# Kernel optimization log

Measured on AMD Instinct MI355X. Metric: run time of the kernel, lower is better.

Reference implementation:

```python
import jax, jax.numpy as jnp
import numpy as np

WIDTH = 1024
HEADS = 16
INIT_SCALE = 0.02


def setup_inputs() -> dict:
    key = jax.random.key(0)
    ks = jax.random.split(key, 5)
    x = jax.random.normal(ks[0], (2, 2048, WIDTH), dtype=jnp.float32)
    # torch Linear weight [out, in]; we store transposed [in, out] for x @ W
    W_qkv = jax.random.normal(ks[1], (WIDTH, 3 * WIDTH), dtype=jnp.float32) * INIT_SCALE
    b_qkv = jnp.zeros((3 * WIDTH,), dtype=jnp.float32)
    W_proj = jax.random.normal(ks[2], (WIDTH, WIDTH), dtype=jnp.float32) * INIT_SCALE
    b_proj = jnp.zeros((WIDTH,), dtype=jnp.float32)
    return {"x": x, "W_qkv": W_qkv, "b_qkv": b_qkv, "W_proj": W_proj, "b_proj": b_proj}


def reference(x, W_qkv, b_qkv, W_proj, b_proj):
    bs, n_ctx, width = x.shape
    heads = HEADS
    attn_ch = width // heads  # per-head channel dim (width*3 // heads // 3)
    scale = 1.0 / np.sqrt(np.sqrt(attn_ch))  # applied to both q and k

    qkv = x @ W_qkv + b_qkv                      # [b, t, 3*width]
    qkv = qkv.reshape(bs, n_ctx, heads, 3 * attn_ch)
    q, k, v = jnp.split(qkv, 3, axis=-1)         # each [b, t, h, c]

    weight = jnp.einsum('bthc,bshc->bhts', q * scale, k * scale)
    wdtype = weight.dtype
    weight = jax.nn.softmax(weight.astype(jnp.float32), axis=-1).astype(wdtype)

    out = jnp.einsum('bhts,bshc->bthc', weight, v).reshape(bs, n_ctx, width)
    return out @ W_proj + b_proj
```

## Files before the change

### kernel.cpp

```cpp
#include <hip/hip_runtime.h>

typedef __attribute__((ext_vector_type(4))) float fx4;
typedef __attribute__((ext_vector_type(16))) float f32x16;
typedef __attribute__((ext_vector_type(8))) short s16x8;
typedef __attribute__((ext_vector_type(2))) unsigned int u32x2;

#define QK_SCALE 0.35355339059327373f
#define LOG2E    1.4426950408889634f

__device__ __forceinline__ short f2bf(float f) {
  union { float f; unsigned int u; } v; v.f = f;
  unsigned int r = v.u + 0x7fffu + ((v.u >> 16) & 1u);
  return (short)(r >> 16);
}

__device__ __forceinline__ unsigned f2u(float f) {
  union { float f; unsigned u; } v; v.f = f; return v.u;
}
__device__ __forceinline__ float u2f(unsigned u) {
  union { unsigned u; float f; } v; v.u = u; return v.f;
}

__device__ __forceinline__ float xhalf_sum(float x) {
  u32x2 r = __builtin_amdgcn_permlane32_swap(f2u(x), f2u(x), false, false);
  return u2f(r[0]) + u2f(r[1]);
}

__device__ __forceinline__ int swz(int row, int cb) {
  return (row * 128 + cb) ^ ((row & 7) << 4);
}

#define GLL(g, lds) __builtin_amdgcn_global_load_lds( \
    (__attribute__((address_space(1))) void*)(void*)(g), \
    (__attribute__((address_space(3))) void*)(void*)(lds), 16, 0, 0)

__global__ __launch_bounds__(256) void prep(
    const float* __restrict__ x, short* __restrict__ x16,
    const float* __restrict__ Wqkv, short* __restrict__ WqkvT,
    const float* __restrict__ Wproj, short* __restrict__ WprojT) {
  const int b = blockIdx.x;
  if (b < 4096) {
    int i = b * 256 + threadIdx.x;
    float4 v = reinterpret_cast<const float4*>(x)[i];
    short4 o;
    o.x = f2bf(v.x); o.y = f2bf(v.y); o.z = f2bf(v.z); o.w = f2bf(v.w);
    reinterpret_cast<short4*>(x16)[i] = o;
    return;
  }
  __shared__ float tile[32][33];
  const float* W; short* WT; int N, bx, by;
  if (b < 7168) { W = Wqkv; WT = WqkvT; N = 3072; int r = b - 4096; bx = r % 96; by = r / 96; }
  else          { W = Wproj; WT = WprojT; N = 1024; int r = b - 7168; bx = r % 32; by = r / 32; }
  const int K = 1024;
  int tx = threadIdx.x & 31, ty = threadIdx.x >> 5;
  int n0 = bx * 32, k0 = by * 32;
#pragma unroll
  for (int i = 0; i < 32; i += 8)
    tile[ty + i][tx] = W[(size_t)(k0 + ty + i) * N + n0 + tx];
  __syncthreads();
#pragma unroll
  for (int i = 0; i < 32; i += 8)
    WT[(size_t)(n0 + ty + i) * K + k0 + tx] = f2bf(tile[tx][ty + i]);
}

template <int MODE, int BK, int BN>
__global__ __launch_bounds__(BN * 4, 4) void gemm_bf16(
    const short* __restrict__ A, const short* __restrict__ Bt,
    const float* __restrict__ bias, float* __restrict__ Cout,
    short* __restrict__ Qo, short* __restrict__ Ko, short* __restrict__ Vo,
    int M, int N, int K) {
  constexpr int T = BN * 4;
  constexpr int NWC = BN / 32;
  constexpr int CA = 16 * BK / T;
  constexpr int CB = BK / 32;
  __shared__ __align__(16) char sA[2][128 * BK * 2];
  __shared__ __align__(16) char sB[2][BN * BK * 2];
  const int tid = threadIdx.x;
  const int w = tid >> 6, l = tid & 63;
  const int lr = l & 15, lg = l >> 4;
  const int bid = blockIdx.x;
  const int m0 = ((bid & 7) * 4 + ((bid >> 3) & 3)) * 128;
  const int n0 = (bid >> 5) * BN;
  const int wr = (w / NWC) * 64, wc = (w % NWC) * 32;

  fx4 accT[2][4] = {};

  auto stage = [&](int kt, int buf) {
#pragma unroll
    for (int i = 0; i < CA; ++i) {
      int c = i * T + tid;
      int r, lch;
      if (BK == 64) { r = c >> 3; lch = (c & 7) ^ (r & 7); }
      else          { r = c >> 2; lch = (c & 3) ^ (r & 3); }
      GLL(A + (size_t)(m0 + r) * K + kt + lch * 8, sA[buf] + c * 16);
    }
#pragma unroll
    for (int i = 0; i < CB; ++i) {
      int c = i * T + tid;
      int r, lch;
      if (BK == 64) { r = c >> 3; lch = (c & 7) ^ (r & 7); }
      else          { r = c >> 2; lch = (c & 3) ^ (r & 3); }
      GLL(Bt + (size_t)(n0 + r) * K + kt + lch * 8, sB[buf] + c * 16);
    }
  };
  auto roff = [&](int R, int kk) {
    return (BK == 64) ? ((R * 128 + kk * 64 + lg * 16) ^ ((R & 7) << 4))
                      : ((R * 64 + lg * 16) ^ ((R & 3) << 4));
  };

  stage(0, 0);
  __syncthreads();

  const int NIT = K / BK;
  int cur = 0;
  for (int it = 0; it < NIT; ++it) {
    if (it + 1 < NIT) stage((it + 1) * BK, cur ^ 1);
#pragma unroll
    for (int kk = 0; kk < (BK == 64 ? 2 : 1); ++kk) {
      s16x8 av[4], bv[2];
#pragma unroll
      for (int m = 0; m < 4; ++m)
        av[m] = *reinterpret_cast<const s16x8*>(sA[cur] + roff(wr + m * 16 + lr, kk));
#pragma unroll
      for (int n = 0; n < 2; ++n)
        bv[n] = *reinterpret_cast<const s16x8*>(sB[cur] + roff(wc + n * 16 + lr, kk));
#pragma unroll
      for (int n = 0; n < 2; ++n)
#pragma unroll
        for (int m = 0; m < 4; ++m)
          accT[n][m] = __builtin_amdgcn_mfma_f32_16x16x32_bf16(bv[n], av[m], accT[n][m], 0, 0, 0);
    }
    __syncthreads();
    cur ^= 1;
  }

#pragma unroll
  for (int n = 0; n < 2; ++n) {
    const int col0 = n0 + wc + n * 16 + lg * 4;
    const float4 bs = *reinterpret_cast<const float4*>(bias + col0);
    if (MODE == 1) {
#pragma unroll
      for (int m = 0; m < 4; ++m) {
        int row = m0 + wr + m * 16 + lr;
        float4 v;
        v.x = accT[n][m][0] + bs.x; v.y = accT[n][m][1] + bs.y;
        v.z = accT[n][m][2] + bs.z; v.w = accT[n][m][3] + bs.w;
        *reinterpret_cast<float4*>(Cout + (size_t)row * N + col0) = v;
      }
    } else {
      const int h = col0 / 192;
      const int rr = col0 - h * 192;
#pragma unroll
      for (int m = 0; m < 4; ++m) {
        int row = m0 + wr + m * 16 + lr;
        int b = row >> 11, t = row & 2047;
        size_t bh = (size_t)b * 16 + h;
        float v0 = accT[n][m][0] + bs.x, v1 = accT[n][m][1] + bs.y;
        float v2 = accT[n][m][2] + bs.z, v3 = accT[n][m][3] + bs.w;
        if (rr < 64) {
          short4 s4;
          s4.x = f2bf(v0 * (QK_SCALE * LOG2E)); s4.y = f2bf(v1 * (QK_SCALE * LOG2E));
          s4.z = f2bf(v2 * (QK_SCALE * LOG2E)); s4.w = f2bf(v3 * (QK_SCALE * LOG2E));
          *reinterpret_cast<short4*>(Qo + (bh * 2048 + t) * 64 + rr) = s4;
        } else if (rr < 128) {
          short4 s4;
          s4.x = f2bf(v0 * QK_SCALE); s4.y = f2bf(v1 * QK_SCALE);
          s4.z = f2bf(v2 * QK_SCALE); s4.w = f2bf(v3 * QK_SCALE);
          *reinterpret_cast<short4*>(Ko + (bh * 2048 + t) * 64 + (rr - 64)) = s4;
        } else {
          Vo[(bh * 64 + (rr - 128) + 0) * 2048 + t] = f2bf(v0);
          Vo[(bh * 64 + (rr - 128) + 1) * 2048 + t] = f2bf(v1);
          Vo[(bh * 64 + (rr - 128) + 2) * 2048 + t] = f2bf(v2);
          Vo[(bh * 64 + (rr - 128) + 3) * 2048 + t] = f2bf(v3);
        }
      }
    }
  }
}

__global__ __launch_bounds__(512, 4) void attn_fwd(
    const short* __restrict__ Q, const short* __restrict__ Kc,
    const short* __restrict__ VT, short* __restrict__ Y) {
  __shared__ __align__(16) char smem[65536];
  const int tid = threadIdx.x;
  const int w = tid >> 6;
  const int wq = w & 3;
  const int half = w >> 2;
  const int t8 = tid & 255;
  const int l = tid & 63;
  const int l31 = l & 31, hi = l >> 5;
  const int bid = blockIdx.x;
  const int bh = (bid & 7) * 4 + ((bid >> 3) & 3);
  const int qt = bid >> 5;
  const int q0 = qt * 128 + wq * 32;
  const int sbase = half * 1024;

  char* kbase = smem + half * 16384;
  char* vbase = smem + 32768 + half * 16384;

  s16x8 qf[4];
  const short* qp = Q + ((size_t)bh * 2048 + q0 + l31) * 64 + hi * 8;
#pragma unroll
  for (int ks = 0; ks < 4; ++ks)
    qf[ks] = *reinterpret_cast<const s16x8*>(qp + ks * 16);

  float lsum = 0.f;
  f32x16 o0 = {}, o1 = {};

#pragma unroll
  for (int i = 0; i < 2; ++i) {
    int c = i * 256 + t8, r = c >> 3, pch = c & 7, lch = pch ^ (r & 7);
    GLL(Kc + ((size_t)bh * 2048 + sbase + r) * 64 + lch * 8, kbase + c * 16);
    GLL(VT + ((size_t)bh * 64 + r) * 2048 + sbase + lch * 8, vbase + c * 16);
  }
  __syncthreads();

  for (int sb = 0; sb < 16; ++sb) {
    const int s0 = sbase + sb * 64;
    if (sb < 15) {
      char* kn = kbase + ((sb + 1) & 1) * 8192;
      char* vn = vbase + ((sb + 1) & 1) * 8192;
#pragma unroll
      for (int i = 0; i < 2; ++i) {
        int c = i * 256 + t8, r = c >> 3, pch = c & 7, lch = pch ^ (r & 7);
        GLL(Kc + ((size_t)bh * 2048 + s0 + 64 + r) * 64 + lch * 8, kn + c * 16);
        GLL(VT + ((size_t)bh * 64 + r) * 2048 + s0 + 64 + lch * 8, vn + c * 16);
      }
    }
    const char* kb = kbase + (sb & 1) * 8192;
    const char* vb = vbase + (sb & 1) * 8192;

    f32x16 p0 = {}, p1 = {};
    __builtin_amdgcn_s_setprio(1);
#pragma unroll
    for (int ks = 0; ks < 4; ++ks) {
      int off = swz(l31, ks * 32 + hi * 16);
      s16x8 ka0 = *reinterpret_cast<const s16x8*>(kb + off);
      s16x8 ka1 = *reinterpret_cast<const s16x8*>(kb + off + 4096);
      p0 = __builtin_amdgcn_mfma_f32_32x32x16_bf16(ka0, qf[ks], p0, 0, 0, 0);
      p1 = __builtin_amdgcn_mfma_f32_32x32x16_bf16(ka1, qf[ks], p1, 0, 0, 0);
    }
    __builtin_amdgcn_s_setprio(0);

#pragma unroll
    for (int i = 0; i < 16; ++i) {
      p0[i] = __builtin_amdgcn_exp2f(p0[i]);
      p1[i] = __builtin_amdgcn_exp2f(p1[i]);
    }
    float s8[8];
#pragma unroll
    for (int i = 0; i < 8; ++i)
      s8[i] = (p0[2 * i] + p0[2 * i + 1]) + (p1[2 * i] + p1[2 * i + 1]);
    lsum += ((s8[0] + s8[1]) + (s8[2] + s8[3])) + ((s8[4] + s8[5]) + (s8[6] + s8[7]));

    int wd[16];
#pragma unroll
    for (int i = 0; i < 8; ++i) {
      asm("v_cvt_pk_bf16_f32 %0, %1, %2" : "=v"(wd[i]) : "v"(p0[2 * i]), "v"(p0[2 * i + 1]));
      asm("v_cvt_pk_bf16_f32 %0, %1, %2" : "=v"(wd[8 + i]) : "v"(p1[2 * i]), "v"(p1[2 * i + 1]));
    }

    __builtin_amdgcn_s_setprio(1);
#pragma unroll
    for (int t = 0; t < 4; ++t) {
      u32x2 s02 = __builtin_amdgcn_permlane32_swap(
          (unsigned)wd[4 * t], (unsigned)wd[4 * t + 2], false, false);
      u32x2 s13 = __builtin_amdgcn_permlane32_swap(
          (unsigned)wd[4 * t + 1], (unsigned)wd[4 * t + 3], false, false);
      union { unsigned i4[4]; s16x8 v; } fr;
      fr.i4[0] = s02[0]; fr.i4[1] = s13[0]; fr.i4[2] = s02[1]; fr.i4[3] = s13[1];
      int off = swz(l31, t * 32 + hi * 16);
      s16x8 v0 = *reinterpret_cast<const s16x8*>(vb + off);
      s16x8 v1 = *reinterpret_cast<const s16x8*>(vb + off + 4096);
      o0 = __builtin_amdgcn_mfma_f32_32x32x16_bf16(v0, fr.v, o0, 0, 0, 0);
      o1 = __builtin_amdgcn_mfma_f32_32x32x16_bf16(v1, fr.v, o1, 0, 0, 0);
    }
    __builtin_amdgcn_s_setprio(0);
    __syncthreads();
  }

  float lt = xhalf_sum(lsum);
  float* scr = (float*)smem;
  float* slsum = (float*)(smem + 32768);
  if (half == 1) {
    float* op = scr + wq * 2048;
#pragma unroll
    for (int gq = 0; gq < 4; ++gq)
#pragma unroll
      for (int j = 0; j < 4; ++j) {
        op[(hi * 4 + 8 * gq + j) * 32 + l31] = o0[4 * gq + j];
        op[(32 + hi * 4 + 8 * gq + j) * 32 + l31] = o1[4 * gq + j];
      }
    if (hi == 0) slsum[wq * 32 + l31] = lt;
  }
  __syncthreads();
  if (half == 0) {
    const int b = bh >> 4, h = bh & 15;
    float inv = 1.f / (lt + slsum[wq * 32 + l31]);
    const float* op = scr + wq * 2048;
    short* yp = Y + ((size_t)b * 2048 + q0 + l31) * 1024 + h * 64 + hi * 4;
#pragma unroll
    for (int gq = 0; gq < 4; ++gq) {
      short4 s4;
      s4.x = f2bf((o0[4 * gq + 0] + op[(hi * 4 + 8 * gq + 0) * 32 + l31]) * inv);
      s4.y = f2bf((o0[4 * gq + 1] + op[(hi * 4 + 8 * gq + 1) * 32 + l31]) * inv);
      s4.z = f2bf((o0[4 * gq + 2] + op[(hi * 4 + 8 * gq + 2) * 32 + l31]) * inv);
      s4.w = f2bf((o0[4 * gq + 3] + op[(hi * 4 + 8 * gq + 3) * 32 + l31]) * inv);
      *reinterpret_cast<short4*>(yp + 8 * gq) = s4;
      s4.x = f2bf((o1[4 * gq + 0] + op[(32 + hi * 4 + 8 * gq + 0) * 32 + l31]) * inv);
      s4.y = f2bf((o1[4 * gq + 1] + op[(32 + hi * 4 + 8 * gq + 1) * 32 + l31]) * inv);
      s4.z = f2bf((o1[4 * gq + 2] + op[(32 + hi * 4 + 8 * gq + 2) * 32 + l31]) * inv);
      s4.w = f2bf((o1[4 * gq + 3] + op[(32 + hi * 4 + 8 * gq + 3) * 32 + l31]) * inv);
      *reinterpret_cast<short4*>(yp + 32 + 8 * gq) = s4;
    }
  }
}

extern "C" void kernel_launch(void* const* d_in, const int* in_sizes, int n_in,
                              void* d_out, int out_size, void* d_ws, size_t ws_size,
                              hipStream_t stream) {
  const float* x     = (const float*)d_in[0];
  const float* Wqkv  = (const float*)d_in[1];
  const float* bqkv  = (const float*)d_in[2];
  const float* Wproj = (const float*)d_in[3];
  const float* bproj = (const float*)d_in[4];
  float* out = (float*)d_out;

  char* ws = (char*)d_ws;
  const size_t MB = 1024 * 1024;
  short* x16    = (short*)(ws);
  short* WqkvT  = (short*)(ws + 8 * MB);
  short* WprojT = (short*)(ws + 14 * MB);
  short* Q16    = (short*)(ws + 16 * MB);
  short* K16    = (short*)(ws + 24 * MB);
  short* VT16   = (short*)(ws + 32 * MB);
  short* Y16    = x16;

  prep<<<8192, 256, 0, stream>>>(x, x16, Wqkv, WqkvT, Wproj, WprojT);
  gemm_bf16<0, 32, 128><<<768, 512, 0, stream>>>(x16, WqkvT, bqkv, nullptr,
                                                 Q16, K16, VT16, 4096, 3072, 1024);
  attn_fwd<<<512, 512, 0, stream>>>(Q16, K16, VT16, Y16);
  gemm_bf16<1, 64, 64><<<512, 256, 0, stream>>>(Y16, WprojT, bproj, out,
                                                nullptr, nullptr, nullptr, 4096, 1024, 1024);
}
```

Baseline: 110.1 us.

## Replace QKV GEMM with 256x256-tile, 4-stage async-copy pipelined kernel

Splits the QKV projection into a dedicated kernel using 256x256 output tiles with BK=32. It streams A and B through a 4-buffer ring in 128KB of dynamic LDS using direct global-to-LDS loads, with XOR swizzling and explicit vmcnt waits. Barriers and setprio are interleaved around the MFMA blocks to overlap loads with compute. The larger tiles raise operand reuse and cut global traffic, but only 192 blocks are launched on a 256-CU device, which risks underusing the GPU.

After: 117.1 us. +6.3%, slower.

```diff
diff --git a/kernel.cpp b/kernel.cpp
--- a/kernel.cpp
+++ b/kernel.cpp
@@ -63,11 +63,128 @@
     WT[(size_t)(n0 + ty + i) * K + k0 + tx] = f2bf(tile[tx][ty + i]);
 }
 
-template <int MODE, int BK, int BN>
-__global__ __launch_bounds__(BN * 4, 4) void gemm_bf16(
+__global__ __launch_bounds__(512, 2) void gemm_qkv(
+    const short* __restrict__ A, const short* __restrict__ Bt,
+    const float* __restrict__ bias,
+    short* __restrict__ Qo, short* __restrict__ Ko, short* __restrict__ Vo) {
+  constexpr int K = 1024;
+  extern __shared__ __align__(16) char smem[];
+  const int tid = threadIdx.x;
+  const int w = tid >> 6, l = tid & 63;
+  const int lr = l & 15, lg = l >> 4;
+  const int wm = w >> 2, wn = w & 3;
+  const int bid = blockIdx.x;
+  const int idx = (bid & 7) * 24 + (bid >> 3);
+  const int m0 = (idx & 15) * 256;
+  const int n0 = (idx >> 4) * 256;
+
+  fx4 accT[4][8] = {};
+
+  auto stageA = [&](int s) {
+    char* dst = smem + (s & 3) * 32768;
+#pragma unroll
+    for (int i = 0; i < 2; ++i) {
+      int c = i * 512 + tid, r = c >> 2, lch = (c & 3) ^ (r & 3);
+      GLL(A + (size_t)(m0 + r) * K + s * 32 + lch * 8, dst + c * 16);
+    }
+  };
+  auto stageB = [&](int s) {
+    char* dst = smem + (s & 3) * 32768 + 16384;
+#pragma unroll
+    for (int i = 0; i < 2; ++i) {
+      int c = i * 512 + tid, r = c >> 2, lch = (c & 3) ^ (r & 3);
+      GLL(Bt + (size_t)(n0 + r) * K + s * 32 + lch * 8, dst + c * 16);
+    }
+  };
+
+  for (int j = 0; j < 3; ++j) { stageA(j); stageB(j); }
+  asm volatile("s_waitcnt vmcnt(8)" ::: "memory");
+  __builtin_amdgcn_s_barrier();
+  __builtin_amdgcn_sched_barrier(0);
+
+  for (int s = 0; s < 32; ++s) {
+    const char* sa = smem + (s & 3) * 32768;
+    const char* sb = sa + 16384;
+    const bool st = (s + 3 < 32);
+    s16x8 bv[4];
+#pragma unroll
+    for (int mh = 0; mh < 2; ++mh) {
+      if (mh == 0) { if (st) stageA(s + 3); }
+      else         { if (st) stageB(s + 3); }
+      s16x8 av[4];
+#pragma unroll
+      for (int mi = 0; mi < 4; ++mi) {
+        int R = wm * 128 + mh * 64 + mi * 16 + lr;
+        av[mi] = *reinterpret_cast<const s16x8*>(sa + ((R * 64 + lg * 16) ^ ((R & 3) << 4)));
+      }
+      if (mh == 0) {
+#pragma unroll
+        for (int n = 0; n < 4; ++n) {
+          int R = wn * 64 + n * 16 + lr;
+          bv[n] = *reinterpret_cast<const s16x8*>(sb + ((R * 64 + lg * 16) ^ ((R & 3) << 4)));
+        }
+      }
+      __builtin_amdgcn_s_barrier();
+      __builtin_amdgcn_sched_barrier(0);
+      __builtin_amdgcn_s_setprio(1);
+#pragma unroll
+      for (int n = 0; n < 4; ++n)
+#pragma unroll
+        for (int mi = 0; mi < 4; ++mi)
+          accT[n][mh * 4 + mi] = __builtin_amdgcn_mfma_f32_16x16x32_bf16(
+              bv[n], av[mi], accT[n][mh * 4 + mi], 0, 0, 0);
+      __builtin_amdgcn_s_setprio(0);
+      if (mh == 0) {
+        __builtin_amdgcn_s_barrier();
+        __builtin_amdgcn_sched_barrier(0);
+      }
+    }
+    if (s < 31) {
+      if (s <= 28)      asm volatile("s_waitcnt vmcnt(8)" ::: "memory");
+      else if (s == 29) asm volatile("s_waitcnt vmcnt(4)" ::: "memory");
+      else              asm volatile("s_waitcnt vmcnt(0)" ::: "memory");
+      __builtin_amdgcn_s_barrier();
+      __builtin_amdgcn_sched_barrier(0);
+    }
+  }
+
+#pragma unroll
+  for (int n = 0; n < 4; ++n) {
+    const int col0 = n0 + wn * 64 + n * 16 + lg * 4;
+    const float4 bs = *reinterpret_cast<const float4*>(bias + col0);
+    const int h = col0 / 192;
+    const int rr = col0 - h * 192;
+#pragma unroll
+    for (int m = 0; m < 8; ++m) {
+      int row = m0 + wm * 128 + m * 16 + lr;
+      int b = row >> 11, t = row & 2047;
+      size_t bh = (size_t)b * 16 + h;
+      float v0 = accT[n][m][0] + bs.x, v1 = accT[n][m][1] + bs.y;
+      float v2 = accT[n][m][2] + bs.z, v3 = accT[n][m][3] + bs.w;
+      if (rr < 64) {
+        short4 s4;
+        s4.x = f2bf(v0 * (QK_SCALE * LOG2E)); s4.y = f2bf(v1 * (QK_SCALE * LOG2E));
+        s4.z = f2bf(v2 * (QK_SCALE * LOG2E)); s4.w = f2bf(v3 * (QK_SCALE * LOG2E));
+        *reinterpret_cast<short4*>(Qo + (bh * 2048 + t) * 64 + rr) = s4;
+      } else if (rr < 128) {
+        short4 s4;
+        s4.x = f2bf(v0 * QK_SCALE); s4.y = f2bf(v1 * QK_SCALE);
+        s4.z = f2bf(v2 * QK_SCALE); s4.w = f2bf(v3 * QK_SCALE);
+        *reinterpret_cast<short4*>(Ko + (bh * 2048 + t) * 64 + (rr - 64)) = s4;
+      } else {
+        Vo[(bh * 64 + (rr - 128) + 0) * 2048 + t] = f2bf(v0);
+        Vo[(bh * 64 + (rr - 128) + 1) * 2048 + t] = f2bf(v1);
+        Vo[(bh * 64 + (rr - 128) + 2) * 2048 + t] = f2bf(v2);
+        Vo[(bh * 64 + (rr - 128) + 3) * 2048 + t] = f2bf(v3);
+      }
+    }
+  }
+}
+
+template <int BK, int BN>
+__global__ __launch_bounds__(BN * 4, 4) void gemm_proj(
     const short* __restrict__ A, const short* __restrict__ Bt,
     const float* __restrict__ bias, float* __restrict__ Cout,
-    short* __restrict__ Qo, short* __restrict__ Ko, short* __restrict__ Vo,
     int M, int N, int K) {
   constexpr int T = BN * 4;
   constexpr int NWC = BN / 32;
@@ -138,42 +255,13 @@
   for (int n = 0; n < 2; ++n) {
     const int col0 = n0 + wc + n * 16 + lg * 4;
     const float4 bs = *reinterpret_cast<const float4*>(bias + col0);
-    if (MODE == 1) {
-#pragma unroll
-      for (int m = 0; m < 4; ++m) {
-        int row = m0 + wr + m * 16 + lr;
-        float4 v;
-        v.x = accT[n][m][0] + bs.x; v.y = accT[n][m][1] + bs.y;
-        v.z = accT[n][m][2] + bs.z; v.w = accT[n][m][3] + bs.w;
-        *reinterpret_cast<float4*>(Cout + (size_t)row * N + col0) = v;
-      }
-    } else {
-      const int h = col0 / 192;
-      const int rr = col0 - h * 192;
-#pragma unroll
-      for (int m = 0; m < 4; ++m) {
-        int row = m0 + wr + m * 16 + lr;
-        int b = row >> 11, t = row & 2047;
-        size_t bh = (size_t)b * 16 + h;
-        float v0 = accT[n][m][0] + bs.x, v1 = accT[n][m][1] + bs.y;
-        float v2 = accT[n][m][2] + bs.z, v3 = accT[n][m][3] + bs.w;
-        if (rr < 64) {
-          short4 s4;
-          s4.x = f2bf(v0 * (QK_SCALE * LOG2E)); s4.y = f2bf(v1 * (QK_SCALE * LOG2E));
-          s4.z = f2bf(v2 * (QK_SCALE * LOG2E)); s4.w = f2bf(v3 * (QK_SCALE * LOG2E));
-          *reinterpret_cast<short4*>(Qo + (bh * 2048 + t) * 64 + rr) = s4;
-        } else if (rr < 128) {
-          short4 s4;
-          s4.x = f2bf(v0 * QK_SCALE); s4.y = f2bf(v1 * QK_SCALE);
-          s4.z = f2bf(v2 * QK_SCALE); s4.w = f2bf(v3 * QK_SCALE);
-          *reinterpret_cast<short4*>(Ko + (bh * 2048 + t) * 64 + (rr - 64)) = s4;
-        } else {
-          Vo[(bh * 64 + (rr - 128) + 0) * 2048 + t] = f2bf(v0);
-          Vo[(bh * 64 + (rr - 128) + 1) * 2048 + t] = f2bf(v1);
-          Vo[(bh * 64 + (rr - 128) + 2) * 2048 + t] = f2bf(v2);
-          Vo[(bh * 64 + (rr - 128) + 3) * 2048 + t] = f2bf(v3);
-        }
-      }
+#pragma unroll
+    for (int m = 0; m < 4; ++m) {
+      int row = m0 + wr + m * 16 + lr;
+      float4 v;
+      v.x = accT[n][m][0] + bs.x; v.y = accT[n][m][1] + bs.y;
+      v.z = accT[n][m][2] + bs.z; v.w = accT[n][m][3] + bs.w;
+      *reinterpret_cast<float4*>(Cout + (size_t)row * N + col0) = v;
     }
   }
 }
@@ -336,10 +424,11 @@
   short* VT16   = (short*)(ws + 32 * MB);
   short* Y16    = x16;
 
+  hipFuncSetAttribute(reinterpret_cast<const void*>(gemm_qkv),
+                      hipFuncAttributeMaxDynamicSharedMemorySize, 131072);
+
   prep<<<8192, 256, 0, stream>>>(x, x16, Wqkv, WqkvT, Wproj, WprojT);
-  gemm_bf16<0, 32, 128><<<768, 512, 0, stream>>>(x16, WqkvT, bqkv, nullptr,
-                                                 Q16, K16, VT16, 4096, 3072, 1024);
+  gemm_qkv<<<192, 512, 131072, stream>>>(x16, WqkvT, bqkv, Q16, K16, VT16);
   attn_fwd<<<512, 512, 0, stream>>>(Q16, K16, VT16, Y16);
-  gemm_bf16<1, 64, 64><<<512, 256, 0, stream>>>(Y16, WprojT, bproj, out,
-                                                nullptr, nullptr, nullptr, 4096, 1024, 1024);
-}
+  gemm_proj<64, 64><<<512, 256, 0, stream>>>(Y16, WprojT, bproj, out, 4096, 1024, 1024);
+}
```
